# Performance work log

Hardware: AMD Instinct MI355X
Metric: run time of the kernel (lower is better)

## Reference

```python
import jax, jax.numpy as jnp
import numpy as np

B, S, C, H, E, K = 8, 512, 768, 12, 8, 2
MLP_H = int(C * 4.0)
HD = C // H
ROUTER_REG = 0.01
LN_EPS = 1e-5


def setup_inputs() -> dict:
    key = jax.random.key(0)
    ks = jax.random.split(key, 8)

    def w(k, shape, fan_in):
        return (jax.random.normal(k, shape, dtype=jnp.float32) / np.sqrt(fan_in)).astype(jnp.float32)

    return {
        "x": jax.random.normal(ks[0], (B, S, C), dtype=jnp.float32),
        "expert_tokens": w(ks[1], (E, C), C),
        "ln1_g": jnp.ones((E, C), jnp.float32),
        "ln1_b": jnp.zeros((E, C), jnp.float32),
        "qkv_w": w(ks[2], (E, C, 3 * C), C),
        "qkv_b": jnp.zeros((E, 3 * C), jnp.float32),
        "proj_w": w(ks[3], (E, C, C), C),
        "proj_b": jnp.zeros((E, C), jnp.float32),
        "ln2_g": jnp.ones((E, C), jnp.float32),
        "ln2_b": jnp.zeros((E, C), jnp.float32),
        "fc1_w": w(ks[4], (E, C, MLP_H), C),
        "fc1_b": jnp.zeros((E, MLP_H), jnp.float32),
        "fc2_w": w(ks[5], (E, MLP_H, C), MLP_H),
        "fc2_b": jnp.zeros((E, C), jnp.float32),
    }


def _layernorm(x, g, b):
    mu = jnp.mean(x, axis=-1, keepdims=True)
    var = jnp.mean(jnp.square(x - mu), axis=-1, keepdims=True)
    return (x - mu) * jax.lax.rsqrt(var + LN_EPS) * g + b


def _block(x, p):
    # One transformer Block (pre-LN attention + MLP), params for a single expert.
    ln1_g, ln1_b, qkv_w, qkv_b, proj_w, proj_b, ln2_g, ln2_b, fc1_w, fc1_b, fc2_w, fc2_b = p
    h = _layernorm(x, ln1_g, ln1_b)
    qkv = (h @ qkv_w + qkv_b).reshape(B, S, 3, H, HD)
    q, k, v = qkv[:, :, 0], qkv[:, :, 1], qkv[:, :, 2]  # [B,S,H,HD]
    # NOTE: original code MULTIPLIES by sqrt(head_dim) (scale = head_dim**0.5).
    scale = jnp.float32(np.sqrt(HD))
    attn = jax.nn.softmax(jnp.einsum('bqhd,bkhd->bhqk', q, k) * scale, axis=-1)
    o = jnp.einsum('bhqk,bkhd->bqhd', attn, v).reshape(B, S, C)
    x = x + (o @ proj_w + proj_b)
    h2 = _layernorm(x, ln2_g, ln2_b)
    x = x + (jax.nn.gelu(h2 @ fc1_w + fc1_b, approximate=False) @ fc2_w + fc2_b)
    return x


def reference(x, expert_tokens, ln1_g, ln1_b, qkv_w, qkv_b, proj_w, proj_b,
              ln2_g, ln2_b, fc1_w, fc1_b, fc2_w, fc2_b):
    # Router
    router_logits = jnp.einsum('bsc,nc->bsn', x, expert_tokens) / jnp.float32(np.sqrt(C))
    router_probs = jax.nn.softmax(router_logits, axis=-1)
    top_k_probs, top_k_idx = jax.lax.top_k(router_probs, K)  # [B,S,K]
    top_k_probs = top_k_probs / jnp.sum(top_k_probs, axis=-1, keepdims=True)

    # Dense all-expert compute (sequential over experts to bound memory)
    params = (ln1_g, ln1_b, qkv_w, qkv_b, proj_w, proj_b, ln2_g, ln2_b,
              fc1_w, fc1_b, fc2_w, fc2_b)
    expert_out = jax.lax.map(lambda p: _block(x, p), params)  # [E,B,S,C]
    expert_out = jnp.transpose(expert_out, (1, 2, 0, 3))       # [B,S,E,C]

    # Top-k gather and weighted combine
    sel = jnp.take_along_axis(expert_out, top_k_idx[..., None], axis=2)  # [B,S,K,C]
    combine = jnp.sum(sel * top_k_probs[..., None], axis=2)
    out = x + combine

    # Load-balance auxiliary loss
    counts = jnp.sum(jax.nn.one_hot(top_k_idx, E, dtype=jnp.float32), axis=(0, 1, 2))
    f_i = counts / jnp.float32(B * S * K)
    P_i = jnp.mean(router_probs, axis=(0, 1))
    balance_loss = E * jnp.sum(f_i * P_i) + ROUTER_REG * jnp.linalg.norm(expert_tokens)
    return out, balance_loss
```

## Files before the change

### kernel.cpp

```cpp
#include <hip/hip_runtime.h>
#include <hip/hip_bf16.h>

#define BB 8
#define SS 512
#define CC 768
#define HH 12
#define HD 64
#define EE 8
#define KK 2
#define MLPH 3072
#define NT (BB*SS)
#define NOUT (NT*CC)

#define SLOTB      68059136ull
#define SLOT_U16   34029568ull
#define SLOT_F32   17014784ull

typedef unsigned int u32;
typedef unsigned short u16;
typedef __attribute__((ext_vector_type(8))) short short8;
typedef __attribute__((ext_vector_type(4))) float f32x4;

__device__ __forceinline__ u16 f2bf(float f) {
    u32 u = __builtin_bit_cast(u32, f);
    u32 r = (u + 0x7fffu + ((u >> 16) & 1u)) >> 16;
    return (u16)r;
}
__device__ __forceinline__ float bf2f(u16 h) {
    u32 u = ((u32)h) << 16;
    return __builtin_bit_cast(float, u);
}
__device__ __forceinline__ void gl_lds16(const void* g, void* l) {
    __builtin_amdgcn_global_load_lds(
        (const __attribute__((address_space(1))) u32*)g,
        (__attribute__((address_space(3))) u32*)l, 16, 0, 0);
}

__device__ __forceinline__ void stage128x64(const u16* __restrict__ G, size_t ldg,
                                            u16* s, int tid)
{
    int wid = tid >> 6, lane = tid & 63;
#pragma unroll
    for (int it = 0; it < 4; ++it) {
        int cb = it * 256 + wid * 64;
        int c = cb + lane;
        int row = c >> 3;
        int ch = (c & 7) ^ (row & 7);
        gl_lds16(G + (size_t)row * ldg + ch * 8, s + cb * 8);
    }
}
__device__ __forceinline__ short8 frag64(const u16* s, int row, int kc, int lb) {
    int ch = (kc * 4 + lb) ^ (row & 7);
    return *(const short8*)(s + row * 64 + ch * 8);
}

__global__ __launch_bounds__(256) void router_kernel(const float* __restrict__ x,
    const float* __restrict__ et, float* __restrict__ W, float* __restrict__ stats)
{
    __shared__ float etl[EE * CC];
    __shared__ float pred[4][2 * EE];
    int tid = threadIdx.x;
    for (int i = tid; i < EE * CC; i += 256) etl[i] = et[i];
    __syncthreads();
    int wid = tid >> 6, lane = tid & 63;
    float psum[EE] = {}, csum[EE] = {};
    for (int i = 0; i < 2; i++) {
        int t = blockIdx.x * 8 + wid * 2 + i;
        const float* xr = x + (size_t)t * CC;
        float acc[EE] = {};
        for (int c = lane; c < CC; c += 64) {
            float xv = xr[c];
#pragma unroll
            for (int e = 0; e < EE; e++) acc[e] += xv * etl[e * CC + c];
        }
#pragma unroll
        for (int e = 0; e < EE; e++)
            for (int off = 1; off < 64; off <<= 1) acc[e] += __shfl_xor(acc[e], off, 64);
        if (lane == 0) {
            const float inv = 0.03608439182435161f;
            float l[EE], m = -1e30f;
#pragma unroll
            for (int e = 0; e < EE; e++) { l[e] = acc[e] * inv; m = fmaxf(m, l[e]); }
            float p[EE], sum = 0.f;
#pragma unroll
            for (int e = 0; e < EE; e++) { p[e] = __expf(l[e] - m); sum += p[e]; }
            int i1 = 0;
#pragma unroll
            for (int e = 1; e < EE; e++) if (p[e] > p[i1]) i1 = e;
            int i2 = -1;
#pragma unroll
            for (int e = 0; e < EE; e++) if (e != i1 && (i2 < 0 || p[e] > p[i2])) i2 = e;
            float wn = p[i1] + p[i2];
#pragma unroll
            for (int e = 0; e < EE; e++) W[t * EE + e] = 0.f;
            W[t * EE + i1] = p[i1] / wn;
            W[t * EE + i2] = p[i2] / wn;
#pragma unroll
            for (int e = 0; e < EE; e++) psum[e] += p[e] / sum;
            csum[i1] += 1.f; csum[i2] += 1.f;
        }
    }
    if (lane == 0) {
#pragma unroll
        for (int e = 0; e < EE; e++) { pred[wid][e] = psum[e]; pred[wid][EE + e] = csum[e]; }
    }
    __syncthreads();
    if (tid < 2 * EE) {
        float s = pred[0][tid] + pred[1][tid] + pred[2][tid] + pred[3][tid];
        atomicAdd(&stats[tid], s);
    }
}

template<int MODE>
__global__ __launch_bounds__(256) void ln_kernel(const float* __restrict__ x, size_t xslot,
    u16* __restrict__ out_hi, u16* __restrict__ out_lo, size_t oslot)
{
    int t = blockIdx.x;
    int eb = blockIdx.y;
    const float* xr = x + (size_t)eb * xslot + (size_t)t * CC;
    __shared__ float red[256];
    int tid = threadIdx.x;
    float v[3];
    float s = 0.f;
#pragma unroll
    for (int i = 0; i < 3; i++) { v[i] = xr[tid + i * 256]; s += v[i]; }
    red[tid] = s; __syncthreads();
    for (int off = 128; off > 0; off >>= 1) { if (tid < off) red[tid] += red[tid + off]; __syncthreads(); }
    float mu = red[0] / (float)CC;
    __syncthreads();
    float s2 = 0.f;
#pragma unroll
    for (int i = 0; i < 3; i++) { float d = v[i] - mu; s2 += d * d; }
    red[tid] = s2; __syncthreads();
    for (int off = 128; off > 0; off >>= 1) { if (tid < off) red[tid] += red[tid + off]; __syncthreads(); }
    float var = red[0] / (float)CC;
    float sc = rsqrtf(var + 1e-5f);
#pragma unroll
    for (int i = 0; i < 3; i++) {
        int c = tid + i * 256;
        float val = (v[i] - mu) * sc;
        u16 hi = f2bf(val);
        out_hi[(size_t)eb * oslot + (size_t)t * CC + c] = hi;
        if (MODE) out_lo[(size_t)eb * oslot + (size_t)t * CC + c] = f2bf(val - bf2f(hi));
    }
}

__global__ __launch_bounds__(256) void prep_expert(
    const float* __restrict__ qkv_w0, const float* __restrict__ qkv_b0,
    const float* __restrict__ proj_w0,
    const float* __restrict__ fc1_w0, const float* __restrict__ fc1_b0,
    const float* __restrict__ fc2_w0,
    const float* __restrict__ g1_0, const float* __restrict__ b1_0,
    const float* __restrict__ g2_0, const float* __restrict__ b2_0,
    u16* __restrict__ qkvTh, u16* __restrict__ qkvTl,
    u16* __restrict__ projT, u16* __restrict__ fc1T, u16* __restrict__ fc2T,
    float* __restrict__ biasq, float* __restrict__ biasf1, int ebase)
{
    __shared__ float tile[32][33];
    __shared__ float bsh[CC];
    __shared__ float redg[256];
    int bid = blockIdx.x;
    int eb = blockIdx.y;
    int ge = ebase + eb;
    int tid = threadIdx.x;
    const float* qkv_w = qkv_w0 + (size_t)ge * CC * 3 * CC;
    const float* qkv_b = qkv_b0 + (size_t)ge * 3 * CC;
    const float* proj_w = proj_w0 + (size_t)ge * CC * CC;
    const float* fc1_w = fc1_w0 + (size_t)ge * CC * MLPH;
    const float* fc1_b = fc1_b0 + (size_t)ge * MLPH;
    const float* fc2_w = fc2_w0 + (size_t)ge * MLPH * CC;
    const float* g1 = g1_0 + (size_t)ge * CC;
    const float* b1 = b1_0 + (size_t)ge * CC;
    const float* g2 = g2_0 + (size_t)ge * CC;
    const float* b2 = b2_0 + (size_t)ge * CC;

    if (bid < 6912) {
        const float* src; const float* scale = nullptr;
        u16 *dh, *dl = nullptr; int N, Kd, n0, k0;
        if (bid < 1728) {
            src = qkv_w; scale = g1;
            dh = qkvTh + (size_t)eb * SLOT_U16; dl = qkvTl + (size_t)eb * SLOT_U16;
            N = 2304; Kd = 768; n0 = (bid % 72) * 32; k0 = (bid / 72) * 32;
        } else if (bid < 2304) {
            int i = bid - 1728;
            src = proj_w; dh = projT + (size_t)eb * SLOT_U16; N = 768; Kd = 768;
            n0 = (i % 24) * 32; k0 = (i / 24) * 32;
        } else if (bid < 4608) {
            int i = bid - 2304;
            src = fc1_w; scale = g2; dh = fc1T + (size_t)eb * SLOT_U16; N = 3072; Kd = 768;
            n0 = (i % 96) * 32; k0 = (i / 96) * 32;
        } else {
            int i = bid - 4608;
            src = fc2_w; dh = fc2T + (size_t)eb * SLOT_U16; N = 768; Kd = 3072;
            n0 = (i % 24) * 32; k0 = (i / 24) * 32;
        }
        int tx = tid & 31, ty = tid >> 5;
#pragma unroll
        for (int i = 0; i < 32; i += 8) {
            float v = src[(size_t)(k0 + ty + i) * N + n0 + tx];
            if (scale) v *= scale[k0 + ty + i];
            tile[ty + i][tx] = v;
        }
        __syncthreads();
#pragma unroll
        for (int i = 0; i < 32; i += 8) {
            float v = tile[tx][ty + i];
            u16 hi = f2bf(v);
            dh[(size_t)(n0 + ty + i) * Kd + k0 + tx] = hi;
            if (dl) dl[(size_t)(n0 + ty + i) * Kd + k0 + tx] = f2bf(v - bf2f(hi));
        }
    } else {
        const float* bv; const float* wsrc; const float* badd;
        float* dst; int N, n0;
        if (bid < 6984) { bv = b1; wsrc = qkv_w; badd = qkv_b; dst = biasq + (size_t)eb * SLOT_F32; N = 2304; n0 = (bid - 6912) * 32; }
        else            { bv = b2; wsrc = fc1_w; badd = fc1_b; dst = biasf1 + (size_t)eb * SLOT_F32; N = MLPH; n0 = (bid - 6984) * 32; }
        for (int i = tid; i < CC; i += 256) bsh[i] = bv[i];
        __syncthreads();
        int g = tid & 31, l8 = tid >> 5;
        int n = n0 + g;
        float acc = 0.f;
        for (int k = l8; k < CC; k += 8) acc += bsh[k] * wsrc[(size_t)k * N + n];
        redg[tid] = acc; __syncthreads();
        if (tid < 32) {
            float sum = 0.f;
#pragma unroll
            for (int i = 0; i < 8; i++) sum += redg[tid + i * 32];
            dst[n0 + tid] = sum + badd[n0 + tid];
        }
    }
}

__global__ __launch_bounds__(256) void gemm_qkv_bk64(
    const u16* __restrict__ Ah, const u16* __restrict__ Al,
    const u16* __restrict__ Bh0, const u16* __restrict__ Bl0,
    const float* __restrict__ biasq0, u16* __restrict__ qk_hi0,
    u16* __restrict__ qk_lo0, u16* __restrict__ vtout0)
{
    __shared__ __align__(16) u16 sAh[128 * 64], sAl[128 * 64];
    __shared__ __align__(16) u16 sBh[128 * 64], sBl[128 * 64];
    int tid = threadIdx.x;
    int eb = blockIdx.z;
    int bm = blockIdx.y * 128, bn = blockIdx.x * 128;
    bool qk_tile = (bn < 1536);
    int wid = tid >> 6, lane = tid & 63;
    int wr = wid >> 1, wc = wid & 1;
    int la = lane & 15, lb = lane >> 4;
    const u16* Bh = Bh0 + (size_t)eb * SLOT_U16;
    const u16* Bl = Bl0 + (size_t)eb * SLOT_U16;
    const float* bias = biasq0 + (size_t)eb * SLOT_F32;
    u16* qk_hi = qk_hi0 + (size_t)eb * SLOT_U16;
    u16* qk_lo = qk_lo0 + (size_t)eb * SLOT_U16;
    u16* vtout = vtout0 + (size_t)eb * SLOT_U16;

    f32x4 acc[4][4];
#pragma unroll
    for (int i = 0; i < 4; i++)
#pragma unroll
        for (int j = 0; j < 4; j++) acc[i][j] = (f32x4){0.f, 0.f, 0.f, 0.f};

    const u16* Abh = Ah + (size_t)bm * CC;
    const u16* Abl = Al + (size_t)bm * CC;
    const u16* Bbh = Bh + (size_t)bn * CC;
    const u16* Bbl = Bl + (size_t)bn * CC;
    for (int k0 = 0; k0 < CC; k0 += 64) {
        stage128x64(Abh + k0, CC, sAh, tid);
        stage128x64(Bbh + k0, CC, sBh, tid);
        if (qk_tile) {
            stage128x64(Abl + k0, CC, sAl, tid);
            stage128x64(Bbl + k0, CC, sBl, tid);
        }
        __syncthreads();
        if (qk_tile) {
#pragma unroll
            for (int kc = 0; kc < 2; kc++) {
                short8 avh[4], avl[4], bvh[4], bvl[4];
#pragma unroll
                for (int i = 0; i < 4; i++) {
                    int row = wr * 64 + i * 16 + la;
                    avh[i] = frag64(sAh, row, kc, lb);
                    avl[i] = frag64(sAl, row, kc, lb);
                }
#pragma unroll
                for (int j = 0; j < 4; j++) {
                    int row = wc * 64 + j * 16 + la;
                    bvh[j] = frag64(sBh, row, kc, lb);
                    bvl[j] = frag64(sBl, row, kc, lb);
                }
#pragma unroll
                for (int i = 0; i < 4; i++)
#pragma unroll
                    for (int j = 0; j < 4; j++) {
                        acc[i][j] = __builtin_amdgcn_mfma_f32_16x16x32_bf16(avh[i], bvh[j], acc[i][j], 0, 0, 0);
                        acc[i][j] = __builtin_amdgcn_mfma_f32_16x16x32_bf16(avh[i], bvl[j], acc[i][j], 0, 0, 0);
                        acc[i][j] = __builtin_amdgcn_mfma_f32_16x16x32_bf16(avl[i], bvh[j], acc[i][j], 0, 0, 0);
                    }
            }
        } else {
#pragma unroll
            for (int kc = 0; kc < 2; kc++) {
                short8 avh[4], bvh[4];
#pragma unroll
                for (int i = 0; i < 4; i++) avh[i] = frag64(sAh, wr * 64 + i * 16 + la, kc, lb);
#pragma unroll
                for (int j = 0; j < 4; j++) bvh[j] = frag64(sBh, wc * 64 + j * 16 + la, kc, lb);
#pragma unroll
                for (int i = 0; i < 4; i++)
#pragma unroll
                    for (int j = 0; j < 4; j++)
                        acc[i][j] = __builtin_amdgcn_mfma_f32_16x16x32_bf16(avh[i], bvh[j], acc[i][j], 0, 0, 0);
            }
        }
        __syncthreads();
    }
#pragma unroll
    for (int i = 0; i < 4; i++) {
#pragma unroll
        for (int j = 0; j < 4; j++) {
            int gn = bn + wc * 64 + j * 16 + la;
            float bsv = bias[gn];
#pragma unroll
            for (int r = 0; r < 4; r++) {
                int gm = bm + wr * 64 + i * 16 + lb * 4 + r;
                float v = acc[i][j][r] + bsv;
                if (gn < 1536) {
                    u16 hi = f2bf(v);
                    qk_hi[(size_t)gm * 1536 + gn] = hi;
                    qk_lo[(size_t)gm * 1536 + gn] = f2bf(v - bf2f(hi));
                } else {
                    int dd = (gn - 1536) & 63, hh = (gn - 1536) >> 6;
                    int ss = gm & (SS - 1), bb = gm >> 9;
                    vtout[((size_t)((bb * HH + hh) * HD + dd)) * SS + ss] = f2bf(v);
                }
            }
        }
    }
}

template<int EPI>
__global__ __launch_bounds__(256) void gemm_b(
    const u16* __restrict__ A, size_t Aslot,
    const u16* __restrict__ BT, size_t Bslot,
    const float* __restrict__ bias, size_t biasSlot,
    const float* __restrict__ res, size_t resSlot,
    const float* __restrict__ Wt, int ebase,
    const float* __restrict__ xinit,
    void* __restrict__ Cout, size_t CoutSlot, int N, int Kdim)
{
    __shared__ __align__(16) u16 sA[128 * 64];
    __shared__ __align__(16) u16 sB[128 * 64];
    int tid = threadIdx.x;
    int eb = blockIdx.z;
    int ge = ebase + eb;
    int bm = blockIdx.y * 128, bn = blockIdx.x * 128;
    int wid = tid >> 6, lane = tid & 63;
    int wr = wid >> 1, wc = wid & 1;
    int la = lane & 15, lb = lane >> 4;
    f32x4 acc[4][4];
#pragma unroll
    for (int i = 0; i < 4; i++)
#pragma unroll
        for (int j = 0; j < 4; j++) acc[i][j] = (f32x4){0.f, 0.f, 0.f, 0.f};

    const u16* Ab = A + (size_t)eb * Aslot + (size_t)bm * Kdim;
    const u16* Bb = BT + (size_t)eb * Bslot + (size_t)bn * Kdim;
    for (int k0 = 0; k0 < Kdim; k0 += 64) {
        stage128x64(Ab + k0, Kdim, sA, tid);
        stage128x64(Bb + k0, Kdim, sB, tid);
        __syncthreads();
#pragma unroll
        for (int kc = 0; kc < 2; kc++) {
            short8 av[4], bv[4];
#pragma unroll
            for (int i = 0; i < 4; i++) av[i] = frag64(sA, wr * 64 + i * 16 + la, kc, lb);
#pragma unroll
            for (int j = 0; j < 4; j++) bv[j] = frag64(sB, wc * 64 + j * 16 + la, kc, lb);
#pragma unroll
            for (int i = 0; i < 4; i++)
#pragma unroll
                for (int j = 0; j < 4; j++)
                    acc[i][j] = __builtin_amdgcn_mfma_f32_16x16x32_bf16(av[i], bv[j], acc[i][j], 0, 0, 0);
        }
        __syncthreads();
    }
    const float* biasp = bias + (size_t)eb * biasSlot;
    const float* resp = res ? res + (size_t)eb * resSlot : nullptr;
#pragma unroll
    for (int i = 0; i < 4; i++) {
#pragma unroll
        for (int j = 0; j < 4; j++) {
            int gn = bn + wc * 64 + j * 16 + la;
            float bsv = biasp[gn];
#pragma unroll
            for (int r = 0; r < 4; r++) {
                int gm = bm + wr * 64 + i * 16 + lb * 4 + r;
                size_t idx = (size_t)gm * N + gn;
                float v = acc[i][j][r];
                if (EPI == 1) {
                    ((float*)Cout + (size_t)eb * CoutSlot)[idx] = resp[idx] + v + bsv;
                } else if (EPI == 2) {
                    v += bsv;
                    float gel = 0.5f * v * (1.0f + erff(v * 0.70710678118654752f));
                    ((u16*)Cout + (size_t)eb * CoutSlot)[idx] = f2bf(gel);
                } else {
                    float w = Wt[(size_t)gm * EE + ge];
                    float val = w * (v + bsv + resp[idx]);
                    if (ge == 0) val += xinit[idx];
                    atomicAdd(&((float*)Cout)[idx], val);
                }
            }
        }
    }
}

__global__ __launch_bounds__(256) void attn_mfma(const u16* __restrict__ qk_hi0,
    const u16* __restrict__ qk_lo0, const u16* __restrict__ vt0, u16* __restrict__ o0)
{
    int q0 = blockIdx.x * 64;
    int h = blockIdx.y;
    int z = blockIdx.z;
    int b = z & (BB - 1), eb = z >> 3;
    int tid = threadIdx.x, wid = tid >> 6, lane = tid & 63;
    int la = lane & 15, lb = lane >> 4;
    __shared__ __align__(16) u16 Ksh[64 * 64];
    __shared__ __align__(16) u16 Ksl[64 * 64];
    __shared__ __align__(16) u16 Vs[64 * 64];
    __shared__ __align__(16) u16 Ps[4][16 * 64];

    const u16* qk_hi = qk_hi0 + (size_t)eb * SLOT_U16;
    const u16* qk_lo = qk_lo0 + (size_t)eb * SLOT_U16;
    const u16* vt = vt0 + (size_t)eb * SLOT_U16;
    u16* o = o0 + (size_t)eb * SLOT_U16;

    short8 aqh[2], aql[2];
    {
        size_t qoff = (size_t)(b * SS + q0 + wid * 16 + la) * 1536 + h * HD;
#pragma unroll
        for (int kc = 0; kc < 2; kc++) {
            aqh[kc] = *(const short8*)(qk_hi + qoff + kc * 32 + lb * 8);
            aql[kc] = *(const short8*)(qk_lo + qoff + kc * 32 + lb * 8);
        }
    }
    const u16* kbh = qk_hi + (size_t)(b * SS) * 1536 + CC + h * HD;
    const u16* kbl = qk_lo + (size_t)(b * SS) * 1536 + CC + h * HD;
    const u16* vtbase = vt + (size_t)((b * HH + h) * HD) * SS;

    float m_r[4], l_r[4];
    f32x4 acc_o[4];
#pragma unroll
    for (int r = 0; r < 4; r++) { m_r[r] = -1e30f; l_r[r] = 0.f; }
#pragma unroll
    for (int d0 = 0; d0 < 4; d0++) acc_o[d0] = (f32x4){0.f, 0.f, 0.f, 0.f};

    for (int kt = 0; kt < SS; kt += 64) {
#pragma unroll
        for (int it = 0; it < 2; it++) {
            int base = it * 256 + wid * 64;
            int c = base + lane;
            int row = c >> 3;
            int gk = (c & 7) ^ (row & 7);
            gl_lds16(kbh + (size_t)(kt + row) * 1536 + gk * 8, Ksh + base * 8);
            gl_lds16(kbl + (size_t)(kt + row) * 1536 + gk * 8, Ksl + base * 8);
            gl_lds16(vtbase + (size_t)row * SS + kt + gk * 8, Vs + base * 8);
        }
        __syncthreads();

        f32x4 s4[4];
#pragma unroll
        for (int j = 0; j < 4; j++) s4[j] = (f32x4){0.f, 0.f, 0.f, 0.f};
#pragma unroll
        for (int kc = 0; kc < 2; kc++)
#pragma unroll
            for (int j = 0; j < 4; j++) {
                size_t off = (size_t)(j * 16 + la) * 64 + (((kc * 4 + lb) ^ (la & 7)) * 8);
                short8 bkh = *(const short8*)(Ksh + off);
                short8 bkl = *(const short8*)(Ksl + off);
                s4[j] = __builtin_amdgcn_mfma_f32_16x16x32_bf16(aqh[kc], bkh, s4[j], 0, 0, 0);
                s4[j] = __builtin_amdgcn_mfma_f32_16x16x32_bf16(aql[kc], bkh, s4[j], 0, 0, 0);
                s4[j] = __builtin_amdgcn_mfma_f32_16x16x32_bf16(aqh[kc], bkl, s4[j], 0, 0, 0);
            }
#pragma unroll
        for (int j = 0; j < 4; j++) s4[j] = s4[j] * 8.f;

#pragma unroll
        for (int r = 0; r < 4; r++) {
            float mx = fmaxf(fmaxf(s4[0][r], s4[1][r]), fmaxf(s4[2][r], s4[3][r]));
#pragma unroll
            for (int off = 1; off < 16; off <<= 1) mx = fmaxf(mx, __shfl_xor(mx, off, 64));
            float mn = fmaxf(m_r[r], mx);
            float corr = __expf(m_r[r] - mn);
            m_r[r] = mn;
            float rs = 0.f;
#pragma unroll
            for (int j = 0; j < 4; j++) {
                float p = __expf(s4[j][r] - mn);
                s4[j][r] = p; rs += p;
            }
#pragma unroll
            for (int off = 1; off < 16; off <<= 1) rs += __shfl_xor(rs, off, 64);
            l_r[r] = l_r[r] * corr + rs;
#pragma unroll
            for (int d0 = 0; d0 < 4; d0++) acc_o[d0][r] = acc_o[d0][r] * corr;
        }
#pragma unroll
        for (int j = 0; j < 4; j++)
#pragma unroll
            for (int r = 0; r < 4; r++) {
                int row = lb * 4 + r;
                int sg = (2 * j + (la >> 3)) ^ (row & 7);
                Ps[wid][row * 64 + sg * 8 + (la & 7)] = f2bf(s4[j][r]);
            }
        short8 pa[2];
#pragma unroll
        for (int kc = 0; kc < 2; kc++)
            pa[kc] = *(const short8*)(&Ps[wid][la * 64 + (((kc * 4 + lb) ^ (la & 7)) * 8)]);
#pragma unroll
        for (int d0 = 0; d0 < 4; d0++)
#pragma unroll
            for (int kc = 0; kc < 2; kc++) {
                short8 bv = *(const short8*)(&Vs[(d0 * 16 + la) * 64 + (((kc * 4 + lb) ^ (la & 7)) * 8)]);
                acc_o[d0] = __builtin_amdgcn_mfma_f32_16x16x32_bf16(pa[kc], bv, acc_o[d0], 0, 0, 0);
            }
        __syncthreads();
    }
#pragma unroll
    for (int r = 0; r < 4; r++) {
        float invl = 1.f / l_r[r];
        int tok = b * SS + q0 + wid * 16 + lb * 4 + r;
#pragma unroll
        for (int d0 = 0; d0 < 4; d0++)
            o[(size_t)tok * CC + h * HD + d0 * 16 + la] = f2bf(acc_o[d0][r] * invl);
    }
}

__global__ __launch_bounds__(256) void loss_kernel(const float* __restrict__ et,
    const float* __restrict__ stats, float* __restrict__ out_loss)
{
    __shared__ float red[256];
    int tid = threadIdx.x;
    float s = 0.f;
    for (int i = tid; i < EE * CC; i += 256) { float v = et[i]; s += v * v; }
    red[tid] = s; __syncthreads();
    for (int off = 128; off > 0; off >>= 1) { if (tid < off) red[tid] += red[tid + off]; __syncthreads(); }
    if (tid == 0) {
        float bl = 0.f;
        for (int e = 0; e < EE; e++) {
            float f = stats[EE + e] / (float)(NT * KK);
            float P = stats[e] / (float)NT;
            bl += f * P;
        }
        *out_loss = (float)EE * bl + 0.01f * sqrtf(red[0]);
    }
}

extern "C" void kernel_launch(void* const* d_in, const int* in_sizes, int n_in,
                              void* d_out, int out_size, void* d_ws, size_t ws_size,
                              hipStream_t stream) {
    const float* x      = (const float*)d_in[0];
    const float* et     = (const float*)d_in[1];
    const float* ln1_g  = (const float*)d_in[2];
    const float* ln1_b  = (const float*)d_in[3];
    const float* qkv_w  = (const float*)d_in[4];
    const float* qkv_b  = (const float*)d_in[5];
    const float* proj_w = (const float*)d_in[6];
    const float* proj_b = (const float*)d_in[7];
    const float* ln2_g  = (const float*)d_in[8];
    const float* ln2_b  = (const float*)d_in[9];
    const float* fc1_w  = (const float*)d_in[10];
    const float* fc1_b  = (const float*)d_in[11];
    const float* fc2_w  = (const float*)d_in[12];
    const float* fc2_b  = (const float*)d_in[13];
    float* outp = (float*)d_out;
    char* base = (char*)d_ws;

    const size_t FIXED = 12714496;
    int EB = 1;
    if (ws_size >= FIXED + 8 * SLOTB) EB = 8;
    else if (ws_size >= FIXED + 4 * SLOTB) EB = 4;
    else if (ws_size >= FIXED + 2 * SLOTB) EB = 2;

    float* W      = (float*)(base);
    float* stats  = (float*)(base + 131072);
    u16*   xh_hi  = (u16*)  (base + 131584);
    u16*   xh_lo  = (u16*)  (base + 6423040);
    char* slot0 = base + FIXED;
    u16*   qkvTh  = (u16*)  (slot0);
    u16*   qkvTl  = (u16*)  (slot0 + 3538944);
    u16*   projT  = (u16*)  (slot0 + 7077888);
    u16*   fc1T   = (u16*)  (slot0 + 8257536);
    u16*   fc2T   = (u16*)  (slot0 + 12976128);
    float* biasq  = (float*)(slot0 + 17694720);
    float* biasf1 = (float*)(slot0 + 17711104);
    u16*   qk_hi  = (u16*)  (slot0 + 17727488);
    u16*   qk_lo  = (u16*)  (slot0 + 30310400);
    u16*   mlp1   = (u16*)  (slot0 + 17727488);
    u16*   vtb    = (u16*)  (slot0 + 42893312);
    u16*   xmhat  = (u16*)  (slot0 + 42893312);
    u16*   obf    = (u16*)  (slot0 + 49184768);
    float* xmid   = (float*)(slot0 + 55476224);

    hipMemsetAsync(stats, 0, 16 * sizeof(float), stream);
    hipMemsetAsync(outp, 0, (size_t)NOUT * sizeof(float), stream);

    router_kernel<<<NT / 8, 256, 0, stream>>>(x, et, W, stats);
    ln_kernel<1><<<dim3(NT, 1), 256, 0, stream>>>(x, 0, xh_hi, xh_lo, 0);

    for (int ebase = 0; ebase < EE; ebase += EB) {
        prep_expert<<<dim3(7080, EB), 256, 0, stream>>>(
            qkv_w, qkv_b, proj_w, fc1_w, fc1_b, fc2_w,
            ln1_g, ln1_b, ln2_g, ln2_b,
            qkvTh, qkvTl, projT, fc1T, fc2T, biasq, biasf1, ebase);

        gemm_qkv_bk64<<<dim3(18, 32, EB), 256, 0, stream>>>(
            xh_hi, xh_lo, qkvTh, qkvTl, biasq, qk_hi, qk_lo, vtb);

        attn_mfma<<<dim3(SS / 64, HH, BB * EB), 256, 0, stream>>>(qk_hi, qk_lo, vtb, obf);

        gemm_b<1><<<dim3(6, 32, EB), 256, 0, stream>>>(
            obf, SLOT_U16, projT, SLOT_U16, proj_b + (size_t)ebase * CC, CC,
            x, 0, nullptr, 0, nullptr, xmid, SLOT_F32, CC, CC);

        ln_kernel<0><<<dim3(NT, EB), 256, 0, stream>>>(xmid, SLOT_F32, xmhat, nullptr, SLOT_U16);

        gemm_b<2><<<dim3(24, 32, EB), 256, 0, stream>>>(
            xmhat, SLOT_U16, fc1T, SLOT_U16, biasf1, SLOT_F32,
            nullptr, 0, nullptr, 0, nullptr, mlp1, SLOT_U16, MLPH, CC);

        gemm_b<5><<<dim3(6, 32, EB), 256, 0, stream>>>(
            mlp1, SLOT_U16, fc2T, SLOT_U16, fc2_b + (size_t)ebase * CC, CC,
            xmid, SLOT_F32, W, ebase, x, outp, 0, CC, MLPH);
    }

    loss_kernel<<<1, 256, 0, stream>>>(et, stats, outp + NOUT);
}
```

Baseline: 1.585 ms.

## Add dedicated 256x128-tile triple-buffered fc1 GEMM kernel with fused GELU

Replaces the generic 128x128 gemm_b<2> launch for the fc1 projection with a specialised 512-thread kernel that computes 256x128 output tiles. It keeps three K-tiles in flight through direct global-to-LDS loads, waits on them with explicit vmcnt counts, and raises wave priority around the MFMA section. Bias and exact-erf GELU stay fused in the epilogue. The larger tile is meant to improve operand reuse and hide load latency, at the cost of more LDS (about 144KB) and registers per block, which lowers occupancy.

```diff
diff --git a/kernel.cpp b/kernel.cpp
--- a/kernel.cpp
+++ b/kernel.cpp
@@ -43,6 +43,20 @@
 #pragma unroll
     for (int it = 0; it < 4; ++it) {
         int cb = it * 256 + wid * 64;
+        int c = cb + lane;
+        int row = c >> 3;
+        int ch = (c & 7) ^ (row & 7);
+        gl_lds16(G + (size_t)row * ldg + ch * 8, s + cb * 8);
+    }
+}
+template<int ROWS>
+__device__ __forceinline__ void stage512(const u16* __restrict__ G, size_t ldg,
+                                         u16* s, int tid)
+{
+    int wid = tid >> 6, lane = tid & 63;
+#pragma unroll
+    for (int it = 0; it < ROWS / 64; ++it) {
+        int cb = it * 512 + wid * 64;
         int c = cb + lane;
         int row = c >> 3;
         int ch = (c & 7) ^ (row & 7);
@@ -397,16 +411,92 @@
                 float v = acc[i][j][r];
                 if (EPI == 1) {
                     ((float*)Cout + (size_t)eb * CoutSlot)[idx] = resp[idx] + v + bsv;
-                } else if (EPI == 2) {
-                    v += bsv;
-                    float gel = 0.5f * v * (1.0f + erff(v * 0.70710678118654752f));
-                    ((u16*)Cout + (size_t)eb * CoutSlot)[idx] = f2bf(gel);
                 } else {
                     float w = Wt[(size_t)gm * EE + ge];
                     float val = w * (v + bsv + resp[idx]);
                     if (ge == 0) val += xinit[idx];
                     atomicAdd(&((float*)Cout)[idx], val);
                 }
+            }
+        }
+    }
+}
+
+__global__ __launch_bounds__(512) void gemm_fc1_256(
+    const u16* __restrict__ A0, const u16* __restrict__ BT0,
+    const float* __restrict__ bias0, u16* __restrict__ Cout0)
+{
+    __shared__ __align__(16) u16 sA[3][256 * 64];
+    __shared__ __align__(16) u16 sB[3][128 * 64];
+    const int NTILE = CC / 64;
+    int tid = threadIdx.x;
+    int eb = blockIdx.z;
+    int bm = blockIdx.y * 256, bn = blockIdx.x * 128;
+    int wid = tid >> 6, lane = tid & 63;
+    int wm = wid >> 1, wn = wid & 1;
+    int la = lane & 15, lb = lane >> 4;
+
+    const u16* Ab = A0 + (size_t)eb * SLOT_U16 + (size_t)bm * CC;
+    const u16* Bb = BT0 + (size_t)eb * SLOT_U16 + (size_t)bn * CC;
+
+    f32x4 acc[4][4];
+#pragma unroll
+    for (int i = 0; i < 4; i++)
+#pragma unroll
+        for (int j = 0; j < 4; j++) acc[i][j] = (f32x4){0.f, 0.f, 0.f, 0.f};
+
+#pragma unroll
+    for (int t = 0; t < 3; t++) {
+        stage512<256>(Ab + t * 64, CC, sA[t], tid);
+        stage512<128>(Bb + t * 64, CC, sB[t], tid);
+    }
+
+    for (int kt = 0; kt < NTILE; ++kt) {
+        if (kt < NTILE - 2)       asm volatile("s_waitcnt vmcnt(12)" ::: "memory");
+        else if (kt == NTILE - 2) asm volatile("s_waitcnt vmcnt(6)" ::: "memory");
+        else                      asm volatile("s_waitcnt vmcnt(0)" ::: "memory");
+        asm volatile("s_barrier" ::: "memory");
+
+        const u16* cA = sA[kt % 3];
+        const u16* cB = sB[kt % 3];
+        __builtin_amdgcn_s_setprio(1);
+#pragma unroll
+        for (int kc = 0; kc < 2; kc++) {
+            short8 av[4], bv[4];
+#pragma unroll
+            for (int i = 0; i < 4; i++) av[i] = frag64(cA, wm * 64 + i * 16 + la, kc, lb);
+#pragma unroll
+            for (int j = 0; j < 4; j++) bv[j] = frag64(cB, wn * 64 + j * 16 + la, kc, lb);
+#pragma unroll
+            for (int i = 0; i < 4; i++)
+#pragma unroll
+                for (int j = 0; j < 4; j++)
+                    acc[i][j] = __builtin_amdgcn_mfma_f32_16x16x32_bf16(av[i], bv[j], acc[i][j], 0, 0, 0);
+        }
+        __builtin_amdgcn_s_setprio(0);
+        asm volatile("s_barrier" ::: "memory");
+
+        int nt = kt + 3;
+        if (nt < NTILE) {
+            stage512<256>(Ab + nt * 64, CC, sA[nt % 3], tid);
+            stage512<128>(Bb + nt * 64, CC, sB[nt % 3], tid);
+        }
+    }
+
+    const float* bp = bias0 + (size_t)eb * SLOT_F32;
+    u16* C = Cout0 + (size_t)eb * SLOT_U16;
+#pragma unroll
+    for (int i = 0; i < 4; i++) {
+#pragma unroll
+        for (int j = 0; j < 4; j++) {
+            int gn = bn + wn * 64 + j * 16 + la;
+            float bsv = bp[gn];
+#pragma unroll
+            for (int r = 0; r < 4; r++) {
+                int gm = bm + wm * 64 + i * 16 + lb * 4 + r;
+                float v = acc[i][j][r] + bsv;
+                float gel = 0.5f * v * (1.0f + erff(v * 0.70710678118654752f));
+                C[(size_t)gm * MLPH + gn] = f2bf(gel);
             }
         }
     }
@@ -621,9 +711,8 @@
 
         ln_kernel<0><<<dim3(NT, EB), 256, 0, stream>>>(xmid, SLOT_F32, xmhat, nullptr, SLOT_U16);
 
-        gemm_b<2><<<dim3(24, 32, EB), 256, 0, stream>>>(
-            xmhat, SLOT_U16, fc1T, SLOT_U16, biasf1, SLOT_F32,
-            nullptr, 0, nullptr, 0, nullptr, mlp1, SLOT_U16, MLPH, CC);
+        gemm_fc1_256<<<dim3(MLPH / 128, NT / 256, EB), 512, 0, stream>>>(
+            xmhat, fc1T, biasf1, mlp1);
 
         gemm_b<5><<<dim3(6, 32, EB), 256, 0, stream>>>(
             mlp1, SLOT_U16, fc2T, SLOT_U16, fc2_b + (size_t)ebase * CC, CC,
```

Result: slower. 1.668 ms (+5.3%).
